# Kernel tuning notes

Measured on AMD Instinct MI355X. Metric: run time of the kernel, lower is better.

The kernel has to match this reference:

```python
import jax, jax.numpy as jnp
import numpy as np

N_NODES = 10000
N_EDGES = 160000
D_IN = 512
D_HID = 1024

def setup_inputs() -> dict:
    key = jax.random.key(0)
    ks = jax.random.split(key, 8)
    feat = jax.random.normal(ks[0], (N_NODES, D_IN), dtype=jnp.float32)
    W1 = jax.random.normal(ks[1], (D_IN, D_HID), dtype=jnp.float32) * (1.0 / np.sqrt(D_IN))
    b1 = jnp.zeros((D_HID,), dtype=jnp.float32)
    W2 = jax.random.normal(ks[2], (D_HID, D_IN), dtype=jnp.float32) * (1.0 / np.sqrt(D_HID))
    b2 = jnp.zeros((D_IN,), dtype=jnp.float32)
    eps = jnp.zeros((1,), dtype=jnp.float32)
    src = jax.random.randint(ks[3], (N_EDGES,), 0, N_NODES, dtype=jnp.int32)
    dst = jax.random.randint(ks[4], (N_EDGES,), 0, N_NODES, dtype=jnp.int32)
    return {"feat": feat, "W1": W1, "b1": b1, "W2": W2, "b2": b2,
            "eps": eps, "src": src, "dst": dst}

def reference(feat, W1, b1, W2, b2, eps, src, dst):
    # message passing: copy src feature along each edge, sum-reduce at dst
    msgs = feat[src]                                   # [E, D_IN] gather
    neigh = jax.ops.segment_sum(msgs, dst, num_segments=feat.shape[0])  # [N, D_IN]
    # GIN combine: (1 + eps) * self + sum(neighbors)
    rst = (1.0 + eps[0]) * feat + neigh
    # apply_func: 2-layer MLP with ReLU
    h = jnp.maximum(rst @ W1 + b1, 0.0)
    h = h @ W2 + b2
    # identity residual (in_dim == out_dim)
    return h + feat
```

## Files before the change

kernel.cpp:

```cpp
#include <hip/hip_runtime.h>

typedef unsigned short u16;
typedef unsigned int u32;
typedef __bf16 bf16x8 __attribute__((ext_vector_type(8)));
typedef float f32x4 __attribute__((ext_vector_type(4)));

#define N_NODES 10000
#define N_EDGES 160000
#define D_IN 512
#define D_HID 1024

#define AS1 __attribute__((address_space(1)))
#define AS3 __attribute__((address_space(3)))

__device__ __forceinline__ u16 f2bf(float f) {
    union { float f; u32 u; } v; v.f = f;
    return (u16)((v.u + 0x7fffu + ((v.u >> 16) & 1u)) >> 16);
}
__device__ __forceinline__ float b2f(u32 h) {
    union { u32 u; float f; } v; v.u = h << 16; return v.f;
}

__global__ void hist_k(const int* __restrict__ dst, int* __restrict__ counts) {
    int e = blockIdx.x * 256 + threadIdx.x;
    if (e < N_EDGES) atomicAdd(&counts[dst[e]], 1);
}

__global__ __launch_bounds__(1024) void scan_k(const int* __restrict__ counts,
                                               int* __restrict__ offs,
                                               int* __restrict__ cursor) {
    __shared__ int wpre[16];
    int t = threadIdx.x, l = t & 63, w = t >> 6;
    int base = t * 10;
    int c[10];
    int lsum = 0;
#pragma unroll
    for (int i = 0; i < 10; i++) {
        int idx = base + i;
        c[i] = (idx < N_NODES) ? counts[idx] : 0;
        lsum += c[i];
    }
    int sc = lsum;
#pragma unroll
    for (int d = 1; d < 64; d <<= 1) {
        int v = __shfl_up(sc, d);
        if (l >= d) sc += v;
    }
    __shared__ int wsum[16];
    if (l == 63) wsum[w] = sc;
    __syncthreads();
    if (w == 0 && l < 16) {
        int v = wsum[l];
        int p = v;
#pragma unroll
        for (int d = 1; d < 16; d <<= 1) {
            int u = __shfl_up(p, d);
            if (l >= d) p += u;
        }
        wpre[l] = p - v;
    }
    __syncthreads();
    int run = wpre[w] + sc - lsum;
#pragma unroll
    for (int i = 0; i < 10; i++) {
        int idx = base + i;
        if (idx < N_NODES) { offs[idx] = run; cursor[idx] = run; run += c[i]; }
    }
    if (t == 1023) offs[N_NODES] = wpre[15] + sc;
}

__global__ void reorder_k(const int* __restrict__ src, const int* __restrict__ dst,
                          int* __restrict__ cursor, int* __restrict__ ssrc) {
    int e = blockIdx.x * 256 + threadIdx.x;
    if (e >= N_EDGES) return;
    int d = dst[e];
    int pos = atomicAdd(&cursor[d], 1);
    ssrc[pos] = src[e];
}

__global__ void cvt_bf16_k(const float* __restrict__ in, u16* __restrict__ out, int n) {
    int i = (blockIdx.x * 256 + threadIdx.x) * 8;
    if (i >= n) return;
    float4 a = *(const float4*)(in + i);
    float4 b = *(const float4*)(in + i + 4);
    uint4 o;
    o.x = (u32)f2bf(a.x) | ((u32)f2bf(a.y) << 16);
    o.y = (u32)f2bf(a.z) | ((u32)f2bf(a.w) << 16);
    o.z = (u32)f2bf(b.x) | ((u32)f2bf(b.y) << 16);
    o.w = (u32)f2bf(b.z) | ((u32)f2bf(b.w) << 16);
    *(uint4*)(out + i) = o;
}

__global__ void transw_k(const float* __restrict__ W1, u16* __restrict__ w1t,
                         const float* __restrict__ W2, u16* __restrict__ w2t) {
    __shared__ float tile[32][33];
    int b = blockIdx.x;
    const float* W; u16* WT; int K, N, nt;
    if (b < 512) { W = W1; WT = w1t; K = D_IN;  N = D_HID; nt = 32; }
    else         { b -= 512; W = W2; WT = w2t; K = D_HID; N = D_IN;  nt = 16; }
    int n0 = (b % nt) * 32, k0 = (b / nt) * 32;
    int tx = threadIdx.x, ty = threadIdx.y;
#pragma unroll
    for (int i = 0; i < 32; i += 8)
        tile[ty + i][tx] = W[(size_t)(k0 + ty + i) * N + n0 + tx];
    __syncthreads();
#pragma unroll
    for (int i = 0; i < 32; i += 8)
        WT[(size_t)(n0 + ty + i) * K + k0 + tx] = f2bf(tile[tx][ty + i]);
}

__global__ __launch_bounds__(128) void gather_k(const float* __restrict__ feat,
                                                const u16* __restrict__ featb,
                                                const float* __restrict__ eps,
                                                const int* __restrict__ offs,
                                                const int* __restrict__ ssrc,
                                                u16* __restrict__ out) {
    int n = (blockIdx.x * 128 + threadIdx.x) >> 6;
    int l = threadIdx.x & 63;
    if (n >= N_NODES) return;
    int beg = offs[n], end = offs[n + 1];
    float s = 1.0f + eps[0];
    float4 s0 = *(const float4*)(feat + (size_t)n * D_IN + l * 8);
    float4 s1 = *(const float4*)(feat + (size_t)n * D_IN + l * 8 + 4);
    float acc[8] = { s * s0.x, s * s0.y, s * s0.z, s * s0.w,
                     s * s1.x, s * s1.y, s * s1.z, s * s1.w };
    int e = beg;
    for (; e + 4 <= end; e += 4) {
        int i0 = ssrc[e], i1 = ssrc[e + 1], i2 = ssrc[e + 2], i3 = ssrc[e + 3];
        uint4 v0 = *(const uint4*)(featb + (size_t)i0 * D_IN + l * 8);
        uint4 v1 = *(const uint4*)(featb + (size_t)i1 * D_IN + l * 8);
        uint4 v2 = *(const uint4*)(featb + (size_t)i2 * D_IN + l * 8);
        uint4 v3 = *(const uint4*)(featb + (size_t)i3 * D_IN + l * 8);
#define ACC4(v) \
        acc[0] += b2f(v.x & 0xffffu); acc[1] += b2f(v.x >> 16); \
        acc[2] += b2f(v.y & 0xffffu); acc[3] += b2f(v.y >> 16); \
        acc[4] += b2f(v.z & 0xffffu); acc[5] += b2f(v.z >> 16); \
        acc[6] += b2f(v.w & 0xffffu); acc[7] += b2f(v.w >> 16);
        ACC4(v0) ACC4(v1) ACC4(v2) ACC4(v3)
    }
    for (; e < end; e++) {
        int i0 = ssrc[e];
        uint4 v0 = *(const uint4*)(featb + (size_t)i0 * D_IN + l * 8);
        ACC4(v0)
    }
#undef ACC4
    uint4 o;
    o.x = (u32)f2bf(acc[0]) | ((u32)f2bf(acc[1]) << 16);
    o.y = (u32)f2bf(acc[2]) | ((u32)f2bf(acc[3]) << 16);
    o.z = (u32)f2bf(acc[4]) | ((u32)f2bf(acc[5]) << 16);
    o.w = (u32)f2bf(acc[6]) | ((u32)f2bf(acc[7]) << 16);
    *(uint4*)(out + (size_t)n * D_IN + l * 8) = o;
}

__global__ __launch_bounds__(1024) void fused_mlp_k(const u16* __restrict__ A,
                                                    const u16* __restrict__ W1T,
                                                    const float* __restrict__ b1,
                                                    const u16* __restrict__ W2T,
                                                    const float* __restrict__ b2,
                                                    const float* __restrict__ feat,
                                                    float* __restrict__ out,
                                                    int M) {
    __shared__ __bf16 sA[48 * 512];
    __shared__ __bf16 sH[48 * 1024];

    int row0 = blockIdx.x * 48;
    if (row0 > M - 48) row0 = M - 48;
    const int t = threadIdx.x;
    const int w = t >> 6, l = t & 63;
    const int lr = l & 15, lq = l >> 4;

#pragma unroll
    for (int q = 0; q < 3; q++) {
        const int row = w * 3 + q;
        const u16* src = A + (size_t)(row0 + row) * 512 + ((l ^ (row & 7)) * 8);
        __builtin_amdgcn_global_load_lds((const AS1 void*)src,
                                         (AS3 void*)(&sA[row * 512]), 16, 0, 0);
    }
    asm volatile("s_waitcnt vmcnt(0)" ::: "memory");
    __syncthreads();

    {
        const int n0 = w * 64;
        f32x4 acc[3][4] = {};
        for (int kt = 0; kt < 8; kt++) {
            bf16x8 fw[2][4];
#pragma unroll
            for (int s = 0; s < 2; s++)
#pragma unroll
                for (int j = 0; j < 4; j++)
                    fw[s][j] = *(const bf16x8*)(W1T + (size_t)(n0 + j * 16 + lr) * 512
                                                + kt * 64 + s * 32 + lq * 8);
#pragma unroll
            for (int s = 0; s < 2; s++) {
                bf16x8 fa[3];
#pragma unroll
                for (int i = 0; i < 3; i++)
                    fa[i] = *(const bf16x8*)(&sA[(i * 16 + lr) * 512
                                             + (((kt * 8 + s * 4 + lq) ^ (lr & 7)) * 8)]);
#pragma unroll
                for (int i = 0; i < 3; i++)
#pragma unroll
                    for (int j = 0; j < 4; j++)
                        acc[i][j] = __builtin_amdgcn_mfma_f32_16x16x32_bf16(
                            fw[s][j], fa[i], acc[i][j], 0, 0, 0);
            }
        }
#pragma unroll
        for (int i = 0; i < 3; i++) {
            const int hrow = i * 16 + lr;
#pragma unroll
            for (int j = 0; j < 4; j++) {
                const int colb = n0 + j * 16 + lq * 4;
                float4 bv = *(const float4*)(b1 + colb);
                float v0 = fmaxf(acc[i][j][0] + bv.x, 0.0f);
                float v1 = fmaxf(acc[i][j][1] + bv.y, 0.0f);
                float v2 = fmaxf(acc[i][j][2] + bv.z, 0.0f);
                float v3 = fmaxf(acc[i][j][3] + bv.w, 0.0f);
                uint2 pv;
                pv.x = (u32)f2bf(v0) | ((u32)f2bf(v1) << 16);
                pv.y = (u32)f2bf(v2) | ((u32)f2bf(v3) << 16);
                const int slot = (colb >> 3) ^ (hrow & 7);
                *(uint2*)((u16*)sH + hrow * 1024 + slot * 8 + (colb & 7)) = pv;
            }
        }
    }
    __syncthreads();

    {
        const int n0 = w * 32;
        f32x4 acc[3][2] = {};
        for (int kt = 0; kt < 16; kt++) {
            bf16x8 fw[2][2];
#pragma unroll
            for (int s = 0; s < 2; s++)
#pragma unroll
                for (int j = 0; j < 2; j++)
                    fw[s][j] = *(const bf16x8*)(W2T + (size_t)(n0 + j * 16 + lr) * 1024
                                                + kt * 64 + s * 32 + lq * 8);
#pragma unroll
            for (int s = 0; s < 2; s++) {
                bf16x8 fh[3];
#pragma unroll
                for (int i = 0; i < 3; i++)
                    fh[i] = *(const bf16x8*)(&sH[(i * 16 + lr) * 1024
                                             + (((kt * 8 + s * 4 + lq) ^ (lr & 7)) * 8)]);
#pragma unroll
                for (int i = 0; i < 3; i++)
#pragma unroll
                    for (int j = 0; j < 2; j++)
                        acc[i][j] = __builtin_amdgcn_mfma_f32_16x16x32_bf16(
                            fw[s][j], fh[i], acc[i][j], 0, 0, 0);
            }
        }
#pragma unroll
        for (int i = 0; i < 3; i++) {
            const int row = row0 + i * 16 + lr;
#pragma unroll
            for (int j = 0; j < 2; j++) {
                const int colb = n0 + j * 16 + lq * 4;
                float4 bv = *(const float4*)(b2 + colb);
                float4 fv = *(const float4*)(feat + (size_t)row * 512 + colb);
                float4 o;
                o.x = acc[i][j][0] + bv.x + fv.x;
                o.y = acc[i][j][1] + bv.y + fv.y;
                o.z = acc[i][j][2] + bv.z + fv.z;
                o.w = acc[i][j][3] + bv.w + fv.w;
                *(float4*)(out + (size_t)row * 512 + colb) = o;
            }
        }
    }
}

extern "C" void kernel_launch(void* const* d_in, const int* in_sizes, int n_in,
                              void* d_out, int out_size, void* d_ws, size_t ws_size,
                              hipStream_t stream) {
    const float* feat = (const float*)d_in[0];
    const float* W1   = (const float*)d_in[1];
    const float* b1   = (const float*)d_in[2];
    const float* W2   = (const float*)d_in[3];
    const float* b2   = (const float*)d_in[4];
    const float* eps  = (const float*)d_in[5];
    const int*   src  = (const int*)d_in[6];
    const int*   dst  = (const int*)d_in[7];
    float* out = (float*)d_out;

    char* ws = (char*)d_ws;
    u16* rst_b16 = (u16*)(ws);
    u16* featb   = (u16*)(ws + 30720000);
    u16* w1t     = (u16*)(ws + 40960000);
    u16* w2t     = (u16*)(ws + 42008576);
    int* counts  = (int*)(ws + 43057152);
    int* offs    = (int*)(ws + 43097152);
    int* cursor  = (int*)(ws + 43137160);
    int* ssrc    = (int*)(ws + 43177160);

    const int NE = N_NODES * D_IN;

    hipMemsetAsync(counts, 0, N_NODES * sizeof(int), stream);
    hist_k<<<(N_EDGES + 255) / 256, 256, 0, stream>>>(dst, counts);
    scan_k<<<1, 1024, 0, stream>>>(counts, offs, cursor);
    reorder_k<<<(N_EDGES + 255) / 256, 256, 0, stream>>>(src, dst, cursor, ssrc);

    cvt_bf16_k<<<NE / 8 / 256, 256, 0, stream>>>(feat, featb, NE);
    transw_k<<<1024, dim3(32, 8), 0, stream>>>(W1, w1t, W2, w2t);

    gather_k<<<(N_NODES + 1) / 2, 128, 0, stream>>>(feat, featb, eps, offs, ssrc, rst_b16);

    const int NB = (N_NODES + 47) / 48;
    fused_mlp_k<<<NB, 1024, 0, stream>>>(rst_b16, w1t, b1, w2t, b2, feat,
                                         out, N_NODES);
}
```

Baseline: 214.7 us.

## Prefetch MLP weight fragments one step ahead and pad LDS rows instead of swizzling

Both GEMM stages of the fused MLP kernel now double-buffer the W1T/W2T register fragments, loading the next k-slice while the current MFMAs run. This is meant to hide global-load latency for the weights. The XOR-swizzled LDS layout for the activation tiles is replaced by padded row strides (520 and 1032 elements), and s_setprio is raised around the MFMA blocks. The explicit vmcnt(0) wait after the LDS-DMA loads is dropped, which could race unless the compiler inserts the wait itself.

New measurement: 213.0 us. Within noise of the previous version (-0.8%).

```diff
diff --git a/kernel.cpp b/kernel.cpp
--- a/kernel.cpp
+++ b/kernel.cpp
@@ -12,6 +12,9 @@
 
 #define AS1 __attribute__((address_space(1)))
 #define AS3 __attribute__((address_space(3)))
+
+#define PA 520
+#define PH 1032
 
 __device__ __forceinline__ u16 f2bf(float f) {
     union { float f; u32 u; } v; v.f = f;
@@ -160,8 +163,8 @@
                                                     const float* __restrict__ feat,
                                                     float* __restrict__ out,
                                                     int M) {
-    __shared__ __bf16 sA[48 * 512];
-    __shared__ __bf16 sH[48 * 1024];
+    __shared__ __bf16 sA[48 * PA];
+    __shared__ __bf16 sH[48 * PH];
 
     int row0 = blockIdx.x * 48;
     if (row0 > M - 48) row0 = M - 48;
@@ -172,37 +175,49 @@
 #pragma unroll
     for (int q = 0; q < 3; q++) {
         const int row = w * 3 + q;
-        const u16* src = A + (size_t)(row0 + row) * 512 + ((l ^ (row & 7)) * 8);
+        const u16* src = A + (size_t)(row0 + row) * 512 + l * 8;
         __builtin_amdgcn_global_load_lds((const AS1 void*)src,
-                                         (AS3 void*)(&sA[row * 512]), 16, 0, 0);
-    }
-    asm volatile("s_waitcnt vmcnt(0)" ::: "memory");
-    __syncthreads();
-
+                                         (AS3 void*)(&sA[row * PA]), 16, 0, 0);
+    }
+    __syncthreads();
+
+    const int n1 = w * 64;
     {
-        const int n0 = w * 64;
+        bf16x8 fw[4];
+#pragma unroll
+        for (int j = 0; j < 4; j++)
+            fw[j] = *(const bf16x8*)(W1T + (size_t)(n1 + j * 16 + lr) * 512 + lq * 8);
+
         f32x4 acc[3][4] = {};
+#pragma unroll 2
         for (int kt = 0; kt < 8; kt++) {
-            bf16x8 fw[2][4];
-#pragma unroll
-            for (int s = 0; s < 2; s++)
-#pragma unroll
-                for (int j = 0; j < 4; j++)
-                    fw[s][j] = *(const bf16x8*)(W1T + (size_t)(n0 + j * 16 + lr) * 512
-                                                + kt * 64 + s * 32 + lq * 8);
 #pragma unroll
             for (int s = 0; s < 2; s++) {
+                bf16x8 fwn[4];
+                const int nkt = s ? kt + 1 : kt;
+                const int ns = s ? 0 : 1;
+                if (nkt < 8) {
+#pragma unroll
+                    for (int j = 0; j < 4; j++)
+                        fwn[j] = *(const bf16x8*)(W1T
+                            + (size_t)(n1 + j * 16 + lr) * 512
+                            + nkt * 64 + ns * 32 + lq * 8);
+                }
                 bf16x8 fa[3];
 #pragma unroll
                 for (int i = 0; i < 3; i++)
-                    fa[i] = *(const bf16x8*)(&sA[(i * 16 + lr) * 512
-                                             + (((kt * 8 + s * 4 + lq) ^ (lr & 7)) * 8)]);
+                    fa[i] = *(const bf16x8*)(&sA[(i * 16 + lr) * PA
+                                             + (kt * 64 + s * 32 + lq * 8)]);
+                __builtin_amdgcn_s_setprio(1);
 #pragma unroll
                 for (int i = 0; i < 3; i++)
 #pragma unroll
                     for (int j = 0; j < 4; j++)
                         acc[i][j] = __builtin_amdgcn_mfma_f32_16x16x32_bf16(
-                            fw[s][j], fa[i], acc[i][j], 0, 0, 0);
+                            fw[j], fa[i], acc[i][j], 0, 0, 0);
+                __builtin_amdgcn_s_setprio(0);
+#pragma unroll
+                for (int j = 0; j < 4; j++) fw[j] = fwn[j];
             }
         }
 #pragma unroll
@@ -210,7 +225,7 @@
             const int hrow = i * 16 + lr;
 #pragma unroll
             for (int j = 0; j < 4; j++) {
-                const int colb = n0 + j * 16 + lq * 4;
+                const int colb = n1 + j * 16 + lq * 4;
                 float4 bv = *(const float4*)(b1 + colb);
                 float v0 = fmaxf(acc[i][j][0] + bv.x, 0.0f);
                 float v1 = fmaxf(acc[i][j][1] + bv.y, 0.0f);
@@ -219,37 +234,49 @@
                 uint2 pv;
                 pv.x = (u32)f2bf(v0) | ((u32)f2bf(v1) << 16);
                 pv.y = (u32)f2bf(v2) | ((u32)f2bf(v3) << 16);
-                const int slot = (colb >> 3) ^ (hrow & 7);
-                *(uint2*)((u16*)sH + hrow * 1024 + slot * 8 + (colb & 7)) = pv;
+                *(uint2*)((u16*)sH + hrow * PH + colb) = pv;
             }
         }
     }
     __syncthreads();
 
+    const int n2 = w * 32;
     {
-        const int n0 = w * 32;
+        bf16x8 gw[2];
+#pragma unroll
+        for (int j = 0; j < 2; j++)
+            gw[j] = *(const bf16x8*)(W2T + (size_t)(n2 + j * 16 + lr) * 1024 + lq * 8);
+
         f32x4 acc[3][2] = {};
+#pragma unroll 2
         for (int kt = 0; kt < 16; kt++) {
-            bf16x8 fw[2][2];
-#pragma unroll
-            for (int s = 0; s < 2; s++)
-#pragma unroll
-                for (int j = 0; j < 2; j++)
-                    fw[s][j] = *(const bf16x8*)(W2T + (size_t)(n0 + j * 16 + lr) * 1024
-                                                + kt * 64 + s * 32 + lq * 8);
 #pragma unroll
             for (int s = 0; s < 2; s++) {
+                bf16x8 gwn[2];
+                const int nkt = s ? kt + 1 : kt;
+                const int ns = s ? 0 : 1;
+                if (nkt < 16) {
+#pragma unroll
+                    for (int j = 0; j < 2; j++)
+                        gwn[j] = *(const bf16x8*)(W2T
+                            + (size_t)(n2 + j * 16 + lr) * 1024
+                            + nkt * 64 + ns * 32 + lq * 8);
+                }
                 bf16x8 fh[3];
 #pragma unroll
                 for (int i = 0; i < 3; i++)
-                    fh[i] = *(const bf16x8*)(&sH[(i * 16 + lr) * 1024
-                                             + (((kt * 8 + s * 4 + lq) ^ (lr & 7)) * 8)]);
+                    fh[i] = *(const bf16x8*)(&sH[(i * 16 + lr) * PH
+                                             + (kt * 64 + s * 32 + lq * 8)]);
+                __builtin_amdgcn_s_setprio(1);
 #pragma unroll
                 for (int i = 0; i < 3; i++)
 #pragma unroll
                     for (int j = 0; j < 2; j++)
                         acc[i][j] = __builtin_amdgcn_mfma_f32_16x16x32_bf16(
-                            fw[s][j], fh[i], acc[i][j], 0, 0, 0);
+                            gw[j], fh[i], acc[i][j], 0, 0, 0);
+                __builtin_amdgcn_s_setprio(0);
+#pragma unroll
+                for (int j = 0; j < 2; j++) gw[j] = gwn[j];
             }
         }
 #pragma unroll
@@ -257,7 +284,7 @@
             const int row = row0 + i * 16 + lr;
 #pragma unroll
             for (int j = 0; j < 2; j++) {
-                const int colb = n0 + j * 16 + lq * 4;
+                const int colb = n2 + j * 16 + lq * 4;
                 float4 bv = *(const float4*)(b2 + colb);
                 float4 fv = *(const float4*)(feat + (size_t)row * 512 + colb);
                 float4 o;
```
